# Kernel tuning notes

Measured on AMD Instinct MI355X. Metric: run time of the kernel, lower is better.

## Reference

```python
import jax, jax.numpy as jnp
import numpy as np
from jax import lax

B, S, H = 1, 2048, 1024
NH, NKV, HD = 16, 4, 64        # heads, kv heads, head_dim = H // NH
I = 3584                        # intermediate size
E, TOPK = 8, 2                  # experts, top-k routing
EPS = 1e-5
THETA = 1e6


def setup_inputs() -> dict:
    key = jax.random.key(0)
    ks = jax.random.split(key, 12)
    sc = 0.02
    return {
        "hidden_states": jax.random.normal(ks[0], (B, S, H), jnp.float32),
        "position_ids": jnp.broadcast_to(jnp.arange(S, dtype=jnp.int32), (B, S)),
        "wq": jax.random.normal(ks[1], (H, NH * HD), jnp.float32) * sc,
        "wk": jax.random.normal(ks[2], (H, NKV * HD), jnp.float32) * sc,
        "wv": jax.random.normal(ks[3], (H, NKV * HD), jnp.float32) * sc,
        "wo": jax.random.normal(ks[4], (NH * HD, H), jnp.float32) * sc,
        "input_norm_w": jnp.ones((H,), jnp.float32),
        "post_norm_w": jnp.ones((H,), jnp.float32),
        "gate_w": jax.random.normal(ks[5], (H, E), jnp.float32) * sc,
        "w1": jax.random.normal(ks[6], (E, H, I), jnp.float32) * sc,
        "w3": jax.random.normal(ks[7], (E, H, I), jnp.float32) * sc,
        "w2": jax.random.normal(ks[8], (E, I, H), jnp.float32) * sc,
    }


def _rmsnorm(x, w):
    var = jnp.mean(jnp.square(x), axis=-1, keepdims=True)
    return x * lax.rsqrt(var + EPS) * w


def _rope(q, k, position_ids):
    # q: [B,S,NH,HD], k: [B,S,NKV,HD]
    inv_freq = 1.0 / (THETA ** (jnp.arange(0, HD, 2, dtype=jnp.float32) / HD))
    freqs = position_ids.astype(jnp.float32)[..., None] * inv_freq  # [B,S,HD/2]
    emb = jnp.concatenate([freqs, freqs], axis=-1)                  # [B,S,HD]
    cos = jnp.cos(emb)[:, :, None, :]
    sin = jnp.sin(emb)[:, :, None, :]

    def rot_half(x):
        x1, x2 = jnp.split(x, 2, axis=-1)
        return jnp.concatenate([-x2, x1], axis=-1)

    return q * cos + rot_half(q) * sin, k * cos + rot_half(k) * sin


def _attention(x, position_ids, wq, wk, wv, wo):
    b, s, _ = x.shape
    q = (x @ wq).reshape(b, s, NH, HD)
    k = (x @ wk).reshape(b, s, NKV, HD)
    v = (x @ wv).reshape(b, s, NKV, HD)
    q, k = _rope(q, k, position_ids)
    groups = NH // NKV
    k = jnp.repeat(k, groups, axis=2)  # [B,S,NH,HD]
    v = jnp.repeat(v, groups, axis=2)
    scale = HD ** -0.5
    scores = jnp.einsum("bqhd,bkhd->bhqk", q, k) * scale
    causal = jnp.tril(jnp.ones((s, s), dtype=bool))
    scores = jnp.where(causal[None, None], scores, jnp.finfo(scores.dtype).min)
    probs = jax.nn.softmax(scores, axis=-1)
    out = jnp.einsum("bhqk,bkhd->bqhd", probs, v).reshape(b, s, NH * HD)
    return out @ wo


def _moe(x, gate_w, w1, w3, w2):
    b, s, h = x.shape
    xt = x.reshape(b * s, h)
    logits = xt @ gate_w                      # [T,E]
    probs = jax.nn.softmax(logits, axis=-1)
    top_w, top_i = lax.top_k(probs, TOPK)     # [T,K]
    top_w = top_w / jnp.sum(top_w, axis=-1, keepdims=True)
    out = jnp.zeros_like(xt)
    for e in range(E):
        we = jnp.sum(jnp.where(top_i == e, top_w, 0.0), axis=-1)   # [T]
        h_e = jax.nn.silu(xt @ w1[e]) * (xt @ w3[e])               # [T,I]
        out = out + we[:, None] * (h_e @ w2[e])
    return out.reshape(b, s, h), logits


def reference(hidden_states, position_ids, wq, wk, wv, wo,
              input_norm_w, post_norm_w, gate_w, w1, w3, w2):
    # MixtralDecoderLayer: norm -> GQA attn -> residual -> norm -> MoE -> residual
    attn_out = _attention(_rmsnorm(hidden_states, input_norm_w),
                          position_ids, wq, wk, wv, wo)
    h = hidden_states + attn_out
    moe_out, _router_logits = _moe(_rmsnorm(h, post_norm_w), gate_w, w1, w3, w2)
    return h + moe_out
```

## Files before the change

### kernel.cpp

```cpp
#include <hip/hip_runtime.h>
#include <math.h>


typedef unsigned short u16;
typedef unsigned int u32;
typedef __attribute__((ext_vector_type(8))) short s16x8;
typedef __attribute__((ext_vector_type(8))) _Float16 f16x8;
typedef __attribute__((ext_vector_type(4))) float f32x4;

#define S_LEN 2048
#define HDIM  1024
#define NHEAD 16
#define NKVH  4
#define HD    64
#define ISZ   3584
#define NEXP  8
#define NSLOT 4096
#define EPS_F 1e-5f
#define NEG_INF -1e30f
#define LOG2E 1.44269504f

__device__ __forceinline__ float bf2f(u16 u) {
    union { u32 i; float f; } c; c.i = ((u32)u) << 16; return c.f;
}
__device__ __forceinline__ u16 f2bf(float f) {
    union { float f; u32 i; } c; c.f = f;
    u32 r = (c.i + 0x7fffu + ((c.i >> 16) & 1u)) >> 16;
    return (u16)r;
}
__device__ __forceinline__ u16 f2h_bits(float f) {
    union { _Float16 h; u16 u; } c; c.h = (_Float16)f; return c.u;
}
__device__ __forceinline__ void async16(const u16* g, u16* l) {
    __builtin_amdgcn_global_load_lds(
        (const __attribute__((address_space(1))) void*)g,
        (__attribute__((address_space(3))) void*)l, 16, 0, 0);
}

__global__ void k_zero_ints(int* __restrict__ p, int n) {
    int i = blockIdx.x * blockDim.x + threadIdx.x;
    if (i < n) p[i] = 0;
}

__global__ __launch_bounds__(256)
void k_rmsnorm_bf(const float* __restrict__ x, const float* __restrict__ w,
                  u16* __restrict__ out) {
    int t = blockIdx.x;
    int tid = threadIdx.x;
    float4 v = ((const float4*)(x + (size_t)t * HDIM))[tid];
    float ss = v.x * v.x + v.y * v.y + v.z * v.z + v.w * v.w;
#pragma unroll
    for (int off = 32; off >= 1; off >>= 1) ss += __shfl_xor(ss, off, 64);
    __shared__ float red[4];
    if ((tid & 63) == 0) red[tid >> 6] = ss;
    __syncthreads();
    float tot = red[0] + red[1] + red[2] + red[3];
    float rstd = rsqrtf(tot * (1.0f / HDIM) + EPS_F);
    float4 wv = ((const float4*)w)[tid];
    uint2 pk;
    pk.x = (u32)f2bf(v.x * rstd * wv.x) | ((u32)f2bf(v.y * rstd * wv.y) << 16);
    pk.y = (u32)f2bf(v.z * rstd * wv.z) | ((u32)f2bf(v.w * rstd * wv.w) << 16);
    ((uint2*)(out + (size_t)t * HDIM))[tid] = pk;
}

__global__ __launch_bounds__(256)
void k_cvt_t(const float* __restrict__ src, u16* __restrict__ dst,
             int R, int C, long long srcZ, long long dstZ) {
    const int z = blockIdx.z;
    src += (size_t)z * srcZ;
    dst += (size_t)z * dstZ;
    const int lane = threadIdx.x & 63, w = threadIdx.x >> 6;
    const int c = blockIdx.x * 64 + lane;
    const int r0 = blockIdx.y * 128 + w * 32;
    float v[32];
#pragma unroll
    for (int i = 0; i < 32; i++) v[i] = src[(size_t)(r0 + i) * C + c];
#pragma unroll
    for (int g = 0; g < 4; g++) {
        uint4 pk;
        pk.x = (u32)f2bf(v[g * 8 + 0]) | ((u32)f2bf(v[g * 8 + 1]) << 16);
        pk.y = (u32)f2bf(v[g * 8 + 2]) | ((u32)f2bf(v[g * 8 + 3]) << 16);
        pk.z = (u32)f2bf(v[g * 8 + 4]) | ((u32)f2bf(v[g * 8 + 5]) << 16);
        pk.w = (u32)f2bf(v[g * 8 + 6]) | ((u32)f2bf(v[g * 8 + 7]) << 16);
        *(uint4*)(&dst[(size_t)c * R + r0 + g * 8]) = pk;
    }
}

__device__ __forceinline__ void stage32(const u16* __restrict__ A,
                                        const u16* __restrict__ Bt, int K,
                                        int rowA0, int rowAmax, int n0, int kc,
                                        u16* buf, int wid, int sr, int sc) {
#pragma unroll
    for (int t = 0; t < 2; t++) {
        int row = wid * 32 + t * 16 + sr;
        int ck = (sc ^ (row & 3)) << 3;
        int ra = rowA0 + row;
        if (ra > rowAmax) ra = rowAmax;
        u16* ldsA = buf + (wid * 32 + t * 16) * 32;
        async16(A + (size_t)ra * K + kc + ck, ldsA);
        async16(Bt + (size_t)(n0 + row) * K + kc + ck, ldsA + 4096);
    }
}

__device__ __forceinline__ void gemm128_dbuf(
    const u16* __restrict__ A, const u16* __restrict__ Bt, int K,
    int kbeg, int kend, int rowA0, int rowAmax, int n0,
    u16* lds, f32x4 acc[4][4]) {
    const int tid = threadIdx.x;
    const int lane = tid & 63, wid = tid >> 6;
    const int sr = lane >> 2, sc = lane & 3;
    const int ln = lane & 15, q = lane >> 4;
    const int wm = wid >> 1, wn = wid & 1;
    stage32(A, Bt, K, rowA0, rowAmax, n0, kbeg, lds, wid, sr, sc);
    int pp = 0;
    for (int kc = kbeg; kc < kend; kc += 32) {
        u16* cur = lds + pp * 8192;
        u16* nxt = lds + (pp ^ 1) * 8192;
        pp ^= 1;
        __syncthreads();
        if (kc + 32 < kend)
            stage32(A, Bt, K, rowA0, rowAmax, n0, kc + 32, nxt, wid, sr, sc);
        s16x8 af[4], bfv[4];
#pragma unroll
        for (int i = 0; i < 4; i++) {
            int ar = wm * 64 + i * 16 + ln;
            af[i] = *(const s16x8*)(cur + ar * 32 + ((q ^ (ar & 3)) << 3));
            int br = wn * 64 + i * 16 + ln;
            bfv[i] = *(const s16x8*)(cur + 4096 + br * 32 + ((q ^ (br & 3)) << 3));
        }
#pragma unroll
        for (int i = 0; i < 4; i++)
#pragma unroll
            for (int j = 0; j < 4; j++)
                acc[i][j] = __builtin_amdgcn_mfma_f32_16x16x32_bf16(
                    af[i], bfv[j], acc[i][j], 0, 0, 0);
    }
}

__global__ __launch_bounds__(256, 2)
void k_gemm_bt(const u16* __restrict__ A, const u16* __restrict__ Bt,
               int M, int N, int K, int mode,
               float* __restrict__ F0, float* __restrict__ F1,
               const float* __restrict__ RES, u16* __restrict__ O16) {
    __shared__ u16 lds[16384];
    const int m0 = blockIdx.y * 128, n0 = blockIdx.x * 128;
    f32x4 acc[4][4];
#pragma unroll
    for (int i = 0; i < 4; i++)
#pragma unroll
        for (int j = 0; j < 4; j++) acc[i][j] = (f32x4){0.f, 0.f, 0.f, 0.f};
    gemm128_dbuf(A, Bt, K, 0, K, m0, M - 1, n0, lds, acc);
    const int lane = threadIdx.x & 63, wid = threadIdx.x >> 6;
    const int ln = lane & 15, q = lane >> 4, wm = wid >> 1, wn = wid & 1;
#pragma unroll
    for (int i = 0; i < 4; i++) {
#pragma unroll
        for (int r = 0; r < 4; r++) {
            int m = m0 + wm * 64 + i * 16 + q * 4 + r;
#pragma unroll
            for (int j = 0; j < 4; j++) {
                int n = n0 + wn * 64 + j * 16 + ln;
                float v = acc[i][j][r];
                if (mode == 0) {
                    F0[(size_t)m * N + n] = v;
                } else if (mode == 1) {
                    O16[(size_t)m * N + n] = f2bf(v);
                } else if (mode == 2) {
                    F0[(size_t)m * N + n] = v + RES[(size_t)m * N + n];
                } else {
                    if (n < 1024)       F0[(size_t)m * 1024 + n] = v;
                    else if (n < 1280)  F1[(size_t)m * 256 + (n - 1024)] = v;
                    else                O16[(size_t)m * 256 + (n - 1280)] = f2h_bits(v);
                }
            }
        }
    }
}

__global__ __launch_bounds__(256, 2)
void k_gemm_bt_moe(const u16* __restrict__ A, const u16* __restrict__ WT,
                   int N, int K, int mode,
                   u16* __restrict__ O16, const u16* __restrict__ AUX,
                   const int* __restrict__ offs) {
    const int e = blockIdx.z;
    const int base = offs[e], cnt = offs[e + 1] - base;
    const int m0 = blockIdx.y * 128;
    if (m0 >= cnt) return;
    __shared__ u16 lds[16384];
    const u16* Bt = WT + (size_t)e * N * K;
    const int n0 = blockIdx.x * 128;
    f32x4 acc[4][4];
#pragma unroll
    for (int i = 0; i < 4; i++)
#pragma unroll
        for (int j = 0; j < 4; j++) acc[i][j] = (f32x4){0.f, 0.f, 0.f, 0.f};
    gemm128_dbuf(A, Bt, K, 0, K, base + m0, NSLOT - 1, n0, lds, acc);
    const int lane = threadIdx.x & 63, wid = threadIdx.x >> 6;
    const int ln = lane & 15, q = lane >> 4, wm = wid >> 1, wn = wid & 1;
#pragma unroll
    for (int i = 0; i < 4; i++) {
#pragma unroll
        for (int r = 0; r < 4; r++) {
            int mloc = wm * 64 + i * 16 + q * 4 + r;
            if (m0 + mloc >= cnt) continue;
            size_t row = (size_t)(base + m0 + mloc);
#pragma unroll
            for (int j = 0; j < 4; j++) {
                int n = n0 + wn * 64 + j * 16 + ln;
                float v = acc[i][j][r];
                if (mode == 1) {
                    O16[row * N + n] = f2bf(v);
                } else {
                    float a = bf2f(AUX[row * N + n]);
                    float s = v / (1.0f + expf(-v));
                    O16[row * N + n] = f2bf(s * a);
                }
            }
        }
    }
}

__global__ __launch_bounds__(256, 2)
void k_moe_w2(const u16* __restrict__ He, const u16* __restrict__ W2T,
              float* __restrict__ OA, float* __restrict__ OB,
              const int* __restrict__ offs) {
    const int z = blockIdx.z;
    const int e = z & 7, half = z >> 3;
    const int base = offs[e], cnt = offs[e + 1] - base;
    const int m0 = blockIdx.y * 128;
    if (m0 >= cnt) return;
    __shared__ u16 lds[16384];
    const u16* Bt = W2T + (size_t)e * HDIM * ISZ;
    const int n0 = blockIdx.x * 128;
    f32x4 acc[4][4];
#pragma unroll
    for (int i = 0; i < 4; i++)
#pragma unroll
        for (int j = 0; j < 4; j++) acc[i][j] = (f32x4){0.f, 0.f, 0.f, 0.f};
    gemm128_dbuf(He, Bt, ISZ, half * (ISZ / 2), (half + 1) * (ISZ / 2),
                 base + m0, NSLOT - 1, n0, lds, acc);
    float* F0 = half ? OB : OA;
    const int lane = threadIdx.x & 63, wid = threadIdx.x >> 6;
    const int ln = lane & 15, q = lane >> 4, wm = wid >> 1, wn = wid & 1;
#pragma unroll
    for (int i = 0; i < 4; i++) {
#pragma unroll
        for (int r = 0; r < 4; r++) {
            int mloc = wm * 64 + i * 16 + q * 4 + r;
            if (m0 + mloc >= cnt) continue;
            size_t row = (size_t)(base + m0 + mloc);
#pragma unroll
            for (int j = 0; j < 4; j++) {
                int n = n0 + wn * 64 + j * 16 + ln;
                F0[row * HDIM + n] = acc[i][j][r];
            }
        }
    }
}

__global__ __launch_bounds__(256)
void k_rope_cvt(const float* __restrict__ q, const float* __restrict__ k,
                const int* __restrict__ pos, u16* __restrict__ qb2,
                u16* __restrict__ kb2) {
    int id = blockIdx.x * blockDim.x + threadIdx.x;
    int d = id & 31;
    int hh = (id >> 5) % (NHEAD + NKVH);
    int s = id / ((NHEAD + NKVH) * 32);
    float p = (float)pos[s];
    float inv = exp2f(-((float)(2 * d) / (float)HD) * log2f(1.0e6f));
    float ang = p * inv;
    float c = cosf(ang), sn = sinf(ang);
    const float* sp; u16* dp;
    if (hh < NHEAD) {
        sp = q + (size_t)s * (NHEAD * HD) + hh * HD;
        dp = qb2 + (size_t)s * (NHEAD * HD) + hh * HD;
    } else {
        sp = k + (size_t)s * (NKVH * HD) + (hh - NHEAD) * HD;
        dp = kb2 + (size_t)s * (NKVH * HD) + (hh - NHEAD) * HD;
    }
    float x1 = sp[d], x2 = sp[d + 32];
    dp[d]      = f2h_bits(x1 * c - x2 * sn);
    dp[d + 32] = f2h_bits(x2 * c + x1 * sn);
}

__global__ __launch_bounds__(256)
void k_attn_mfma(const u16* __restrict__ qb, const u16* __restrict__ kb,
                 const u16* __restrict__ vb, u16* __restrict__ ob) {
    __shared__ u16 Qs[64 * 64];
    __shared__ u16 Ks[64 * 64];
    __shared__ u16 Vt[64 * 64];
    __shared__ u16 Ps[64 * 64];
    const int qt = blockIdx.x, h = blockIdx.y, kvh = h >> 2;
    const int tid = threadIdx.x, lane = tid & 63, w = tid >> 6;
    const int ln = lane & 15, quad = lane >> 4;

#pragma unroll
    for (int p = 0; p < 2; p++) {
        int r = p * 32 + (tid >> 3), c = tid & 7;
        uint4 v = *(const uint4*)(qb + (size_t)(qt * 64 + r) * (NHEAD * HD) +
                                  h * HD + c * 8);
        *(uint4*)&Qs[r * 64 + ((c ^ (r & 7)) << 3)] = v;
    }

    float m_[4], l_[4];
    f32x4 Oa[4];
#pragma unroll
    for (int r = 0; r < 4; r++) { m_[r] = NEG_INF; l_[r] = 0.0f; }
#pragma unroll
    for (int nt = 0; nt < 4; nt++) Oa[nt] = (f32x4){0.f, 0.f, 0.f, 0.f};

    for (int kt = 0; kt <= qt; kt++) {
        __syncthreads();
#pragma unroll
        for (int p = 0; p < 2; p++) {
            int r = p * 32 + (tid >> 3), c = tid & 7;
            uint4 v = *(const uint4*)(kb + (size_t)(kt * 64 + r) * (NKVH * HD) +
                                      kvh * HD + c * 8);
            *(uint4*)&Ks[r * 64 + ((c ^ (r & 7)) << 3)] = v;
        }
        {
            int s = tid & 63;
#pragma unroll
            for (int half = 0; half < 2; half++) {
                int d0 = w * 16 + half * 8;
                uint4 v = *(const uint4*)(vb + (size_t)(kt * 64 + s) * (NKVH * HD) +
                                          kvh * HD + d0);
                u16 a[8];
                a[0] = (u16)(v.x & 0xffff); a[1] = (u16)(v.x >> 16);
                a[2] = (u16)(v.y & 0xffff); a[3] = (u16)(v.y >> 16);
                a[4] = (u16)(v.z & 0xffff); a[5] = (u16)(v.z >> 16);
                a[6] = (u16)(v.w & 0xffff); a[7] = (u16)(v.w >> 16);
#pragma unroll
                for (int j = 0; j < 8; j++) {
                    int d = d0 + j;
                    Vt[d * 64 + (((s >> 3) ^ (d & 7)) << 3) + (s & 7)] = a[j];
                }
            }
        }
        __syncthreads();

        f32x4 sc[4];
#pragma unroll
        for (int nt = 0; nt < 4; nt++) sc[nt] = (f32x4){0.f, 0.f, 0.f, 0.f};
#pragma unroll
        for (int ks = 0; ks < 2; ks++) {
            int arow = 16 * w + ln;
            f16x8 af = *(const f16x8*)&Qs[arow * 64 +
                                          (((ks * 4 + quad) ^ (arow & 7)) << 3)];
#pragma unroll
            for (int nt = 0; nt < 4; nt++) {
                int brow = nt * 16 + ln;
                f16x8 bf = *(const f16x8*)&Ks[brow * 64 +
                                              (((ks * 4 + quad) ^ (brow & 7)) << 3)];
                sc[nt] = __builtin_amdgcn_mfma_f32_16x16x32_f16(af, bf, sc[nt],
                                                                0, 0, 0);
            }
        }

        const bool diag = (kt == qt);
        float mt[4];
#pragma unroll
        for (int r = 0; r < 4; r++) {
            int qrow = quad * 4 + r + 16 * w;
#pragma unroll
            for (int nt = 0; nt < 4; nt++) {
                float s = sc[nt][r] * 0.125f;
                if (diag && (nt * 16 + ln) > qrow) s = NEG_INF;
                sc[nt][r] = s;
            }
            mt[r] = fmaxf(fmaxf(sc[0][r], sc[1][r]), fmaxf(sc[2][r], sc[3][r]));
        }
#pragma unroll
        for (int off = 8; off >= 1; off >>= 1)
#pragma unroll
            for (int r = 0; r < 4; r++)
                mt[r] = fmaxf(mt[r], __shfl_xor(mt[r], off, 64));

        float rs[4];
#pragma unroll
        for (int r = 0; r < 4; r++) {
            float mn = fmaxf(m_[r], mt[r]);
            float al = exp2f((m_[r] - mn) * LOG2E);
            m_[r] = mn;
            float acc0 = 0.0f;
#pragma unroll
            for (int nt = 0; nt < 4; nt++) {
                float pv = exp2f((sc[nt][r] - mn) * LOG2E);
                sc[nt][r] = pv;
                acc0 += pv;
            }
            rs[r] = acc0;
            l_[r] *= al;
#pragma unroll
            for (int nt = 0; nt < 4; nt++) Oa[nt][r] *= al;
        }
#pragma unroll
        for (int off = 8; off >= 1; off >>= 1)
#pragma unroll
            for (int r = 0; r < 4; r++) rs[r] += __shfl_xor(rs[r], off, 64);
#pragma unroll
        for (int r = 0; r < 4; r++) l_[r] += rs[r];

#pragma unroll
        for (int r = 0; r < 4; r++) {
            int row = 16 * w + quad * 4 + r;
#pragma unroll
            for (int nt = 0; nt < 4; nt++) {
                int ch = nt * 2 + (ln >> 3);
                Ps[row * 64 + ((ch ^ (row & 7)) << 3) + (ln & 7)] =
                    f2h_bits(sc[nt][r]);
            }
        }
        __syncthreads();

#pragma unroll
        for (int ks = 0; ks < 2; ks++) {
            int arow = 16 * w + ln;
            f16x8 pf = *(const f16x8*)&Ps[arow * 64 +
                                          (((ks * 4 + quad) ^ (arow & 7)) << 3)];
#pragma unroll
            for (int nt = 0; nt < 4; nt++) {
                int vrow = nt * 16 + ln;
                f16x8 vf = *(const f16x8*)&Vt[vrow * 64 +
                                              (((ks * 4 + quad) ^ (vrow & 7)) << 3)];
                Oa[nt] = __builtin_amdgcn_mfma_f32_16x16x32_f16(pf, vf, Oa[nt],
                                                                0, 0, 0);
            }
        }
    }

#pragma unroll
    for (int r = 0; r < 4; r++) {
        float inv = 1.0f / l_[r];
        int sg = qt * 64 + 16 * w + quad * 4 + r;
#pragma unroll
        for (int nt = 0; nt < 4; nt++) {
            int d = nt * 16 + ln;
            ob[(size_t)sg * HDIM + h * HD + d] = f2bf(Oa[nt][r] * inv);
        }
    }
}

__global__ __launch_bounds__(64)
void k_gate(const float* __restrict__ Hst, const float* __restrict__ PW,
            const float* __restrict__ GW, int* __restrict__ cnt,
            int* __restrict__ top_i, float* __restrict__ top_w) {
    int t = blockIdx.x;
    int lane = threadIdx.x;
    const float* hrow = Hst + (size_t)t * HDIM;
    float ss = 0.0f;
    float acc[NEXP] = {};
    for (int hh = lane; hh < HDIM; hh += 64) {
        float hv = hrow[hh];
        ss += hv * hv;
        float xw = hv * PW[hh];
        const float* g = GW + (size_t)hh * NEXP;
#pragma unroll
        for (int e = 0; e < NEXP; e++) acc[e] += xw * g[e];
    }
#pragma unroll
    for (int off = 32; off >= 1; off >>= 1) {
        ss += __shfl_xor(ss, off, 64);
#pragma unroll
        for (int e = 0; e < NEXP; e++) acc[e] += __shfl_xor(acc[e], off, 64);
    }
    if (lane == 0) {
        float rstd = rsqrtf(ss * (1.0f / HDIM) + EPS_F);
        int e0 = 0;
        for (int e = 1; e < NEXP; e++) if (acc[e] > acc[e0]) e0 = e;
        int e1 = (e0 == 0) ? 1 : 0;
        for (int e = 0; e < NEXP; e++)
            if (e != e0 && acc[e] > acc[e1]) e1 = e;
        float w0 = 1.0f / (1.0f + expf((acc[e1] - acc[e0]) * rstd));
        top_i[t * 2 + 0] = e0; top_i[t * 2 + 1] = e1;
        top_w[t * 2 + 0] = w0; top_w[t * 2 + 1] = 1.0f - w0;
        atomicAdd(&cnt[e0], 1);
        atomicAdd(&cnt[e1], 1);
    }
}

__global__ void k_prefix(const int* __restrict__ cnt, int* __restrict__ offs,
                         int* __restrict__ cur) {
    if (blockIdx.x == 0 && threadIdx.x == 0) {
        int a = 0;
        for (int e = 0; e < NEXP; e++) { offs[e] = a; cur[e] = a; a += cnt[e]; }
        offs[NEXP] = a;
    }
}

__global__ __launch_bounds__(256)
void k_fill(const int* __restrict__ top_i, int* __restrict__ cur,
            int* __restrict__ idxg, int* __restrict__ slot) {
    int t = blockIdx.x * blockDim.x + threadIdx.x;
    if (t >= S_LEN) return;
#pragma unroll
    for (int kk = 0; kk < 2; kk++) {
        int e = top_i[t * 2 + kk];
        int p = atomicAdd(&cur[e], 1);
        idxg[p] = t;
        slot[t * 2 + kk] = p;
    }
}

__global__ __launch_bounds__(256)
void k_gather(const u16* __restrict__ xnb, const int* __restrict__ idxg,
              u16* __restrict__ Xg) {
    int p = blockIdx.x;
    int t = idxg[p];
    const uint2* s = (const uint2*)(xnb + (size_t)t * HDIM);
    uint2* d = (uint2*)(Xg + (size_t)p * HDIM);
    d[threadIdx.x] = s[threadIdx.x];
}

__global__ __launch_bounds__(256)
void k_combine2(const float* __restrict__ OA, const float* __restrict__ OB,
                const int* __restrict__ slot, const float* __restrict__ top_w,
                float* __restrict__ out) {
    int t = blockIdx.x, tid = threadIdx.x;
    int s0 = slot[t * 2], s1 = slot[t * 2 + 1];
    float w0 = top_w[t * 2], w1 = top_w[t * 2 + 1];
    float4 a0 = ((const float4*)(OA + (size_t)s0 * HDIM))[tid];
    float4 b0 = ((const float4*)(OB + (size_t)s0 * HDIM))[tid];
    float4 a1 = ((const float4*)(OA + (size_t)s1 * HDIM))[tid];
    float4 b1 = ((const float4*)(OB + (size_t)s1 * HDIM))[tid];
    float4* o = (float4*)(out + (size_t)t * HDIM);
    float4 c = o[tid];
    c.x += w0 * (a0.x + b0.x) + w1 * (a1.x + b1.x);
    c.y += w0 * (a0.y + b0.y) + w1 * (a1.y + b1.y);
    c.z += w0 * (a0.z + b0.z) + w1 * (a1.z + b1.z);
    c.w += w0 * (a0.w + b0.w) + w1 * (a1.w + b1.w);
    o[tid] = c;
}

extern "C" void kernel_launch(void* const* d_in, const int* in_sizes, int n_in,
                              void* d_out, int out_size, void* d_ws,
                              size_t ws_size, hipStream_t stream) {
    (void)in_sizes; (void)n_in; (void)out_size; (void)ws_size;
    const float* hidden = (const float*)d_in[0];
    const int*   pos    = (const int*)d_in[1];
    const float* wq     = (const float*)d_in[2];
    const float* wk     = (const float*)d_in[3];
    const float* wv     = (const float*)d_in[4];
    const float* wo     = (const float*)d_in[5];
    const float* innw   = (const float*)d_in[6];
    const float* postnw = (const float*)d_in[7];
    const float* gatew  = (const float*)d_in[8];
    const float* w1     = (const float*)d_in[9];
    const float* w3     = (const float*)d_in[10];
    const float* w2     = (const float*)d_in[11];
    float* out = (float*)d_out;

    u16* w1t  = (u16*)d_ws;
    u16* w3t  = w1t + (size_t)NEXP * ISZ * HDIM;
    u16* w2t  = w3t + (size_t)NEXP * ISZ * HDIM;
    u16* qkvt = w2t + (size_t)NEXP * ISZ * HDIM;
    u16* wot  = qkvt + (size_t)1536 * HDIM;
    u16* xnb  = wot + (size_t)HDIM * HDIM;
    float* qbuf = (float*)(xnb + (size_t)S_LEN * HDIM);
    float* kbuf = qbuf + (size_t)S_LEN * HDIM;
    u16* vb16   = (u16*)(kbuf + (size_t)S_LEN * NKVH * HD);
    u16* qb2    = vb16 + (size_t)S_LEN * NKVH * HD;
    u16* kb2    = qb2 + (size_t)S_LEN * HDIM;
    u16* attnb  = kb2 + (size_t)S_LEN * NKVH * HD;
    float* oexpA = qbuf;
    u16* Xg  = attnb + (size_t)S_LEN * HDIM;
    u16* hg3 = Xg + (size_t)NSLOT * HDIM;
    u16* he  = hg3 + (size_t)NSLOT * ISZ;
    float* oexpB = (float*)(he + (size_t)NSLOT * ISZ);
    int* ib  = (int*)(oexpB + (size_t)NSLOT * HDIM);
    int*   cnt   = ib;
    int*   offs  = ib + 16;
    int*   cur   = ib + 32;
    int*   top_i = ib + 64;
    int*   slot  = ib + 64 + 4096;
    int*   idxg  = ib + 64 + 8192;
    float* top_w = (float*)(ib + 64 + 12288);

    const long long HI = (long long)HDIM * ISZ;

    k_zero_ints<<<1, 64, 0, stream>>>(cnt, 64);
    k_rmsnorm_bf<<<S_LEN, 256, 0, stream>>>(hidden, innw, xnb);

    k_cvt_t<<<dim3(16, 8, 1), 256, 0, stream>>>(wq, qkvt, 1024, 1024, 0, 0);
    k_cvt_t<<<dim3(4, 8, 1), 256, 0, stream>>>(wk, qkvt + (size_t)1024 * 1024, 1024, 256, 0, 0);
    k_cvt_t<<<dim3(4, 8, 1), 256, 0, stream>>>(wv, qkvt + (size_t)1280 * 1024, 1024, 256, 0, 0);
    k_cvt_t<<<dim3(16, 8, 1), 256, 0, stream>>>(wo, wot, 1024, 1024, 0, 0);
    k_cvt_t<<<dim3(56, 8, NEXP), 256, 0, stream>>>(w1, w1t, 1024, 3584, HI, HI);
    k_cvt_t<<<dim3(56, 8, NEXP), 256, 0, stream>>>(w3, w3t, 1024, 3584, HI, HI);
    k_cvt_t<<<dim3(16, 28, NEXP), 256, 0, stream>>>(w2, w2t, 3584, 1024, HI, HI);

    k_gemm_bt<<<dim3(12, 16), 256, 0, stream>>>(xnb, qkvt, 2048, 1536, 1024, 3,
                                                qbuf, kbuf, nullptr, vb16);
    k_rope_cvt<<<(S_LEN * (NHEAD + NKVH) * 32) / 256, 256, 0, stream>>>(
        qbuf, kbuf, pos, qb2, kb2);
    k_attn_mfma<<<dim3(32, 16), 256, 0, stream>>>(qb2, kb2, vb16, attnb);
    k_gemm_bt<<<dim3(8, 16), 256, 0, stream>>>(attnb, wot, 2048, 1024, 1024, 2,
                                               out, nullptr, hidden, nullptr);
    k_rmsnorm_bf<<<S_LEN, 256, 0, stream>>>(out, postnw, xnb);
    k_gate<<<S_LEN, 64, 0, stream>>>(out, postnw, gatew, cnt, top_i, top_w);
    k_prefix<<<1, 1, 0, stream>>>(cnt, offs, cur);
    k_fill<<<S_LEN / 256, 256, 0, stream>>>(top_i, cur, idxg, slot);
    k_gather<<<NSLOT, 256, 0, stream>>>(xnb, idxg, Xg);

    k_gemm_bt_moe<<<dim3(28, 16, NEXP), 256, 0, stream>>>(Xg, w3t, 3584, 1024, 1,
                                                          hg3, nullptr, offs);
    k_gemm_bt_moe<<<dim3(28, 16, NEXP), 256, 0, stream>>>(Xg, w1t, 3584, 1024, 2,
                                                          he, hg3, offs);
    k_moe_w2<<<dim3(8, 16, 16), 256, 0, stream>>>(he, w2t, oexpA, oexpB, offs);
    k_combine2<<<S_LEN, 256, 0, stream>>>(oexpA, oexpB, slot, top_w, out);
}
```

Before: 919.9 us.

## Fuse MoE W1 and W3 GEMMs into one kernel with shared A tile

Replaces the two separate expert GEMMs (W3 written to a bf16 intermediate, then W1 reading it back for SiLU-multiply) with a single kernel that computes both accumulators from one shared staged X tile and applies SiLU(x·W1)·(x·W3) in the epilogue. This removes the intermediate hg3 round trip through global memory, halves the A-tile loads, and drops one launch. Block indices are also remapped from a flat 1D grid so that consecutive N-blocks of the same expert land on the same XCD, for L2 reuse. In exchange the kernel doubles its accumulator registers (32 f32x4) and uses 48KB of LDS, which may reduce occupancy below the requested 2 blocks per CU.

```diff
diff --git a/kernel.cpp b/kernel.cpp
--- a/kernel.cpp
+++ b/kernel.cpp
@@ -99,6 +99,25 @@
         u16* ldsA = buf + (wid * 32 + t * 16) * 32;
         async16(A + (size_t)ra * K + kc + ck, ldsA);
         async16(Bt + (size_t)(n0 + row) * K + kc + ck, ldsA + 4096);
+    }
+}
+
+__device__ __forceinline__ void stage32_w13(const u16* __restrict__ A,
+                                            const u16* __restrict__ B1,
+                                            const u16* __restrict__ B3, int K,
+                                            int rowA0, int rowAmax, int n0,
+                                            int kc, u16* buf, int wid, int sr,
+                                            int sc) {
+#pragma unroll
+    for (int t = 0; t < 2; t++) {
+        int row = wid * 32 + t * 16 + sr;
+        int ck = (sc ^ (row & 3)) << 3;
+        int ra = rowA0 + row;
+        if (ra > rowAmax) ra = rowAmax;
+        u16* ldsA = buf + (wid * 32 + t * 16) * 32;
+        async16(A + (size_t)ra * K + kc + ck, ldsA);
+        async16(B1 + (size_t)(n0 + row) * K + kc + ck, ldsA + 4096);
+        async16(B3 + (size_t)(n0 + row) * K + kc + ck, ldsA + 8192);
     }
 }
 
@@ -178,25 +197,68 @@
 }
 
 __global__ __launch_bounds__(256, 2)
-void k_gemm_bt_moe(const u16* __restrict__ A, const u16* __restrict__ WT,
-                   int N, int K, int mode,
-                   u16* __restrict__ O16, const u16* __restrict__ AUX,
-                   const int* __restrict__ offs) {
-    const int e = blockIdx.z;
+void k_moe_w13(const u16* __restrict__ Xg, const u16* __restrict__ W1T,
+               const u16* __restrict__ W3T, u16* __restrict__ He,
+               const int* __restrict__ offs) {
+    const int bid = blockIdx.x;
+    const int xcd = bid & 7;
+    const int r_ = bid >> 3;
+    const int mb = r_ & 15;
+    const int gslot = r_ >> 4;
+    const int gid = gslot * 8 + xcd;
+    const int e = gid / 28;
+    const int nb = gid - e * 28;
     const int base = offs[e], cnt = offs[e + 1] - base;
-    const int m0 = blockIdx.y * 128;
+    const int m0 = mb * 128;
     if (m0 >= cnt) return;
-    __shared__ u16 lds[16384];
-    const u16* Bt = WT + (size_t)e * N * K;
-    const int n0 = blockIdx.x * 128;
-    f32x4 acc[4][4];
+    __shared__ u16 lds[24576];
+    const u16* B1 = W1T + (size_t)e * ISZ * HDIM;
+    const u16* B3 = W3T + (size_t)e * ISZ * HDIM;
+    const int n0 = nb * 128;
+    f32x4 acc1[4][4], acc3[4][4];
 #pragma unroll
     for (int i = 0; i < 4; i++)
 #pragma unroll
-        for (int j = 0; j < 4; j++) acc[i][j] = (f32x4){0.f, 0.f, 0.f, 0.f};
-    gemm128_dbuf(A, Bt, K, 0, K, base + m0, NSLOT - 1, n0, lds, acc);
-    const int lane = threadIdx.x & 63, wid = threadIdx.x >> 6;
-    const int ln = lane & 15, q = lane >> 4, wm = wid >> 1, wn = wid & 1;
+        for (int j = 0; j < 4; j++) {
+            acc1[i][j] = (f32x4){0.f, 0.f, 0.f, 0.f};
+            acc3[i][j] = (f32x4){0.f, 0.f, 0.f, 0.f};
+        }
+    const int tid = threadIdx.x;
+    const int lane = tid & 63, wid = tid >> 6;
+    const int sr = lane >> 2, sc = lane & 3;
+    const int ln = lane & 15, q = lane >> 4;
+    const int wm = wid >> 1, wn = wid & 1;
+    const int rowA0 = base + m0;
+    stage32_w13(Xg, B1, B3, HDIM, rowA0, NSLOT - 1, n0, 0, lds, wid, sr, sc);
+    int pp = 0;
+    for (int kc = 0; kc < HDIM; kc += 32) {
+        u16* cur = lds + pp * 12288;
+        u16* nxt = lds + (pp ^ 1) * 12288;
+        pp ^= 1;
+        __syncthreads();
+        if (kc + 32 < HDIM)
+            stage32_w13(Xg, B1, B3, HDIM, rowA0, NSLOT - 1, n0, kc + 32, nxt,
+                        wid, sr, sc);
+        s16x8 af[4], b1f[4], b3f[4];
+#pragma unroll
+        for (int i = 0; i < 4; i++) {
+            int ar = wm * 64 + i * 16 + ln;
+            af[i] = *(const s16x8*)(cur + ar * 32 + ((q ^ (ar & 3)) << 3));
+            int br = wn * 64 + i * 16 + ln;
+            int bo = br * 32 + ((q ^ (br & 3)) << 3);
+            b1f[i] = *(const s16x8*)(cur + 4096 + bo);
+            b3f[i] = *(const s16x8*)(cur + 8192 + bo);
+        }
+#pragma unroll
+        for (int i = 0; i < 4; i++)
+#pragma unroll
+            for (int j = 0; j < 4; j++) {
+                acc1[i][j] = __builtin_amdgcn_mfma_f32_16x16x32_bf16(
+                    af[i], b1f[j], acc1[i][j], 0, 0, 0);
+                acc3[i][j] = __builtin_amdgcn_mfma_f32_16x16x32_bf16(
+                    af[i], b3f[j], acc3[i][j], 0, 0, 0);
+            }
+    }
 #pragma unroll
     for (int i = 0; i < 4; i++) {
 #pragma unroll
@@ -207,14 +269,10 @@
 #pragma unroll
             for (int j = 0; j < 4; j++) {
                 int n = n0 + wn * 64 + j * 16 + ln;
-                float v = acc[i][j][r];
-                if (mode == 1) {
-                    O16[row * N + n] = f2bf(v);
-                } else {
-                    float a = bf2f(AUX[row * N + n]);
-                    float s = v / (1.0f + expf(-v));
-                    O16[row * N + n] = f2bf(s * a);
-                }
+                float v1 = acc1[i][j][r];
+                float v3 = acc3[i][j][r];
+                float s = v1 / (1.0f + expf(-v1));
+                He[row * ISZ + n] = f2bf(s * v3);
             }
         }
     }
@@ -602,10 +660,7 @@
     k_fill<<<S_LEN / 256, 256, 0, stream>>>(top_i, cur, idxg, slot);
     k_gather<<<NSLOT, 256, 0, stream>>>(xnb, idxg, Xg);
 
-    k_gemm_bt_moe<<<dim3(28, 16, NEXP), 256, 0, stream>>>(Xg, w3t, 3584, 1024, 1,
-                                                          hg3, nullptr, offs);
-    k_gemm_bt_moe<<<dim3(28, 16, NEXP), 256, 0, stream>>>(Xg, w1t, 3584, 1024, 2,
-                                                          he, hg3, offs);
+    k_moe_w13<<<dim3(28 * 16 * NEXP), 256, 0, stream>>>(Xg, w1t, w3t, he, offs);
     k_moe_w2<<<dim3(8, 16, 16), 256, 0, stream>>>(he, w2t, oexpA, oexpB, offs);
     k_combine2<<<S_LEN, 256, 0, stream>>>(oexpA, oexpB, slot, top_w, out);
 }
```

Result: faster. 883.4 us (-4.0%).
